# Optimization experiments

Measured on AMD Instinct MI355X. Metric: run time of the kernel, lower is better.

## Reference

```python
import jax, jax.numpy as jnp
import numpy as np

B, N, NVT, HS, GS, NZ, TE = 512, 32, 32, 512, 1024, 56, 3


def setup_inputs() -> dict:
    key = jax.random.key(0)
    ks = jax.random.split(key, 18)
    def w(k, shape, fan_in):
        return (jax.random.normal(k, shape, jnp.float32) / np.sqrt(fan_in)).astype(jnp.float32)
    node_types = jax.random.randint(ks[0], (B, N), 0, NVT, dtype=jnp.int32)
    # strictly upper-triangular random DAG: adj[b,u,v]=1 means edge u->v, u<v
    adj = ((jax.random.uniform(ks[1], (B, N, N)) < 0.15)
           & (jnp.triu(jnp.ones((N, N), bool), 1))).astype(jnp.float32)
    return {
        'node_types': node_types,
        'adj': adj,
        'finit_w': w(ks[2], (NVT + GS, HS), NVT + GS),
        'finit_b': w(ks[3], (HS,), HS),
        'fe_w':    w(ks[4], (2 * HS + 1, 2 * HS), 2 * HS + 1),
        'fe_b':    w(ks[5], (2 * HS,), 2 * HS),
        'grue_wih': w(ks[6], (TE, 3 * HS, 2 * HS), 2 * HS),
        'grue_whh': w(ks[7], (TE, 3 * HS, HS), HS),
        'grue_bih': w(ks[8], (TE, 3 * HS), HS),
        'grue_bhh': w(ks[9], (TE, 3 * HS), HS),
        'gate_w':  w(ks[10], (HS, GS), HS),
        'gate_b':  w(ks[11], (GS,), HS),
        'mapper_w': w(ks[12], (HS, GS), HS),
        'fc1_w':   w(ks[13], (GS, NZ), GS),
        'fc1_b':   w(ks[14], (NZ,), GS),
        'fc2_w':   w(ks[15], (GS, NZ), GS),
        'fc2_b':   w(ks[16], (NZ,), GS),
    }


def reference(node_types, adj, finit_w, finit_b, fe_w, fe_b,
              grue_wih, grue_whh, grue_bih, grue_bhh,
              gate_w, gate_b, mapper_w, fc1_w, fc1_b, fc2_w, fc2_b):
    # --- vertex init: finit(cat([one_hot(type), zeros(gs)])) -> only first NVT rows of finit_w matter
    X = jax.nn.one_hot(node_types, NVT, dtype=adj.dtype)          # [B,N,nvt]
    H = X @ finit_w[:NVT] + finit_b                                # [B,N,hs]

    deg = adj.sum(1)                                               # [B,N] in-degree of v
    # torch skips the fe+GRU update for vertex v only if NO graph in batch has a pred at v
    has_pred = (adj.sum((0, 1)) > 0)[None, :, None]                # [1,N,1]

    # fe(cat([H_u, e=1, H_v])) decomposed: W_nei@H_u + w_e + W_self@H_v + b, summed over preds
    Wn, we, Ws = fe_w[:HS], fe_w[HS], fe_w[HS + 1:]

    def step(H, p):
        wih, whh, bih, bhh = p
        Hu = H @ Wn                                                # [B,N,2hs]
        self_t = H @ Ws + we + fe_b                                # [B,N,2hs]
        # Av[b,v] = sum_u adj[b,u,v]*Hu[b,u] + deg[b,v]*self_t[b,v]
        Av = jnp.einsum('buv,bue->bve', adj, Hu) + deg[..., None] * self_t
        gx = Av @ wih.T + bih                                      # [B,N,3hs]
        gh = H @ whh.T + bhh                                       # [B,N,3hs]
        xr, xz, xn = jnp.split(gx, 3, -1)
        hr, hz, hn = jnp.split(gh, 3, -1)
        r = jax.nn.sigmoid(xr + hr)
        z = jax.nn.sigmoid(xz + hz)
        n = jnp.tanh(xn + r * hn)
        Hn = (1.0 - z) * n + z * H                                 # torch GRUCell
        return jnp.where(has_pred, Hn, H), None

    H, _ = jax.lax.scan(step, H, (grue_wih, grue_whh, grue_bih, grue_bhh))

    # gated graph readout: sum_v sigmoid(gate(Hv)) * mapper(Hv)
    Hg = (jax.nn.sigmoid(H @ gate_w + gate_b) * (H @ mapper_w)).sum(1)  # [B,gs]
    mu = Hg @ fc1_w + fc1_b
    logvar = Hg @ fc2_w + fc2_b
    return jnp.stack([mu, logvar], 0)                              # [2,B,nz]
```

## Files before the change

kernel.cpp:

```cpp
#include <hip/hip_runtime.h>
#include <hip/hip_bf16.h>

namespace {

constexpr int kB = 512, kN = 32, kHS = 512, kHS2 = 1024, kHS3 = 1536;
constexpr int kGS = 1024, kNZ = 56, kTE = 3;

typedef __attribute__((ext_vector_type(8))) short bf16x8;
typedef __attribute__((ext_vector_type(4))) float f32x4;

__device__ inline ushort f2bf(float f) {
    union { float f; unsigned u; } v; v.f = f;
    unsigned r = v.u + 0x7fffu + ((v.u >> 16) & 1u);
    return (ushort)(r >> 16);
}
__device__ inline float bf2f(ushort b) {
    union { unsigned u; float f; } v; v.u = ((unsigned)b) << 16;
    return v.f;
}

__global__ __launch_bounds__(256) void wnst_kernel(const float* __restrict__ fe_w,
    ushort* __restrict__ out)
{
    int idx = blockIdx.x * 256 + threadIdx.x;
    int n = idx >> 9, k = idx & 511;
    float v = (n < kHS2) ? fe_w[(size_t)k * kHS2 + n]
                         : fe_w[(size_t)(kHS + 1 + k) * kHS2 + (n - kHS2)];
    out[idx] = f2bf(v);
}

__global__ __launch_bounds__(256) void gatemap_kernel(const float* __restrict__ gw,
    const float* __restrict__ mw, ushort* __restrict__ out)
{
    int idx = blockIdx.x * 256 + threadIdx.x;
    int n = idx >> 9, k = idx & 511;
    float v = (n < kGS) ? gw[(size_t)k * kGS + n] : mw[(size_t)k * kGS + (n - kGS)];
    out[idx] = f2bf(v);
}

__global__ __launch_bounds__(256) void catrzn_kernel(const float* __restrict__ wih,
    const float* __restrict__ whh, ushort* __restrict__ out)
{
    int k = blockIdx.x * 256 + threadIdx.x;
    int n = blockIdx.y, t = blockIdx.z;
    float v;
    if (k < kHS2)       v = wih[((size_t)t * kHS3 + n) * kHS2 + k];
    else if (n < kHS2)  v = whh[((size_t)t * kHS3 + n) * kHS + (k - kHS2)];
    else                v = 0.f;
    out[((size_t)t * kHS3 + n) * kHS3 + k] = f2bf(v);
}

__global__ __launch_bounds__(256) void whhn_kernel(const float* __restrict__ whh,
    ushort* __restrict__ out)
{
    int k = blockIdx.x * 256 + threadIdx.x;
    int n = blockIdx.y, t = blockIdx.z;
    out[((size_t)t * kHS + n) * kHS + k] =
        f2bf(whh[((size_t)t * kHS3 + kHS2 + n) * kHS + k]);
}

__global__ __launch_bounds__(256) void deg_kernel(const float* __restrict__ adj,
    float* __restrict__ deg)
{
    int idx = blockIdx.x * 256 + threadIdx.x;
    int b = idx >> 5, v = idx & 31;
    const float* p = adj + (size_t)b * kN * kN + v;
    float s = 0.f;
    #pragma unroll
    for (int u = 0; u < kN; ++u) s += p[u * kN];
    deg[idx] = s;
}

__global__ void haspred_kernel(const float* __restrict__ deg, int* __restrict__ hp)
{
    int v = threadIdx.x;
    float s = 0.f;
    for (int b = 0; b < kB; ++b) s += deg[b * kN + v];
    hp[v] = (s > 0.f) ? 1 : 0;
}

__global__ void biasHS_kernel(const float* __restrict__ fe_w,
    const float* __restrict__ fe_b, float* __restrict__ o)
{
    int e = blockIdx.x * 256 + threadIdx.x;
    o[e] = (e < kHS2) ? 0.f
                      : fe_w[(size_t)kHS * kHS2 + (e - kHS2)] + fe_b[e - kHS2];
}

__global__ void biasGXN_kernel(const float* __restrict__ bih,
    const float* __restrict__ bhh, float* __restrict__ o)
{
    int idx = blockIdx.x * 256 + threadIdx.x;
    int t = idx / kHS3, e = idx % kHS3;
    float v = bih[t * kHS3 + e];
    if (e < kHS2) v += bhh[t * kHS3 + e];
    o[idx] = v;
}

__global__ void biasRO_kernel(const float* __restrict__ gb, float* __restrict__ o)
{
    int e = blockIdx.x * 256 + threadIdx.x;
    o[e] = (e < kGS) ? gb[e] : 0.f;
}

__global__ __launch_bounds__(256) void hinit_kernel(const int* __restrict__ nt,
    const float* __restrict__ finit_w, const float* __restrict__ finit_b,
    ushort* __restrict__ AvH)
{
    int idx = blockIdx.x * 256 + threadIdx.x;
    int m = idx >> 9;
    int h = idx & 511;
    int t = nt[m];
    AvH[(size_t)m * kHS3 + kHS2 + h] = f2bf(finit_w[t * kHS + h] + finit_b[h]);
}

template<typename CT>
__global__ __launch_bounds__(256, 2) void gemm_bf16(const ushort* __restrict__ A,
    const ushort* __restrict__ B, CT* __restrict__ C,
    const float* __restrict__ bias, int M_, int N_, int K_, int lda)
{
    __shared__ ushort smem[3 * 12288];
    const int tid = threadIdx.x;
    const int w = tid >> 6, l = tid & 63;
    const int l15 = l & 15;

    int nwg = gridDim.x * gridDim.y;
    int bid = blockIdx.y * gridDim.x + blockIdx.x;
    int swz = (nwg & 7) ? bid : ((bid & 7) * (nwg >> 3) + (bid >> 3));
    const int bx = swz % gridDim.x, by = swz / gridDim.x;
    const int mT = by * 128, nT = bx * 256;

    const int NT = K_ >> 5;

    auto stage = [&](const ushort* G, int ldg, int rowOff, int buf, int aOff,
                     int idx, int kt2) {
        int row = idx >> 2, sl = idx & 3;
        int gs = sl ^ ((row >> 1) & 3);
        const ushort* g = G + (size_t)(rowOff + row) * ldg + kt2 + gs * 8;
        __builtin_amdgcn_global_load_lds(
            (const __attribute__((address_space(1))) void*)g,
            (__attribute__((address_space(3))) void*)(smem + buf * 12288 + aOff + idx * 8),
            16, 0, 0);
    };
    auto stage_ph0 = [&](int t) {
        int buf = t % 3, kt2 = t * 32;
        stage(A, lda, mT, buf, 0, tid, kt2);
        stage(A, lda, mT, buf, 0, 256 + tid, kt2);
        stage(B, K_, nT, buf, 4096, tid, kt2);
    };
    auto stage_ph1 = [&](int t) {
        int buf = t % 3, kt2 = t * 32;
        stage(B, K_, nT, buf, 4096, 256 + tid, kt2);
        stage(B, K_, nT, buf, 4096, 512 + tid, kt2);
        stage(B, K_, nT, buf, 4096, 768 + tid, kt2);
    };

    f32x4 acc[8][4] = {};
    bf16x8 bfr[4];
    const int swd = ((l >> 4) ^ (l15 >> 1)) & 3;

    stage_ph0(0); stage_ph1(0);
    stage_ph0(1); stage_ph1(1);

    for (int t = 0; t < NT; ++t) {
        if (t + 1 < NT) asm volatile("s_waitcnt vmcnt(6)" ::: "memory");
        else            asm volatile("s_waitcnt vmcnt(0)" ::: "memory");
        __builtin_amdgcn_s_barrier();

        const ushort* Ab = smem + (t % 3) * 12288;
        const ushort* Bb = Ab + 4096;
        const bool st = (t + 2 < NT);

        bf16x8 af[4];
        #pragma unroll
        for (int i = 0; i < 4; ++i)
            af[i] = *reinterpret_cast<const bf16x8*>(
                &Ab[(i * 16 + l15) * 32 + swd * 8]);
        #pragma unroll
        for (int j = 0; j < 4; ++j)
            bfr[j] = *reinterpret_cast<const bf16x8*>(
                &Bb[(w * 64 + j * 16 + l15) * 32 + swd * 8]);
        if (st) stage_ph0(t + 2);
        asm volatile("s_waitcnt lgkmcnt(0)" ::: "memory");
        __builtin_amdgcn_sched_barrier(0);
        __builtin_amdgcn_s_setprio(1);
        #pragma unroll
        for (int i = 0; i < 4; ++i)
            #pragma unroll
            for (int j = 0; j < 4; ++j)
                acc[i][j] = __builtin_amdgcn_mfma_f32_16x16x32_bf16(
                    af[i], bfr[j], acc[i][j], 0, 0, 0);
        __builtin_amdgcn_s_setprio(0);
        __builtin_amdgcn_s_barrier();

        #pragma unroll
        for (int i = 0; i < 4; ++i)
            af[i] = *reinterpret_cast<const bf16x8*>(
                &Ab[((4 + i) * 16 + l15) * 32 + swd * 8]);
        if (st) stage_ph1(t + 2);
        asm volatile("s_waitcnt lgkmcnt(0)" ::: "memory");
        __builtin_amdgcn_sched_barrier(0);
        __builtin_amdgcn_s_setprio(1);
        #pragma unroll
        for (int i = 0; i < 4; ++i)
            #pragma unroll
            for (int j = 0; j < 4; ++j)
                acc[4 + i][j] = __builtin_amdgcn_mfma_f32_16x16x32_bf16(
                    af[i], bfr[j], acc[4 + i][j], 0, 0, 0);
        __builtin_amdgcn_s_setprio(0);
        __builtin_amdgcn_s_barrier();
    }

    const int row0 = (l >> 4) * 4;
    #pragma unroll
    for (int ni = 0; ni < 4; ++ni) {
        int col = nT + w * 64 + ni * 16 + l15;
        float bv = bias ? bias[col] : 0.f;
        #pragma unroll
        for (int mi = 0; mi < 8; ++mi) {
            #pragma unroll
            for (int q = 0; q < 4; ++q) {
                int row = mT + mi * 16 + row0 + q;
                float val = acc[mi][ni][q] + bv;
                if constexpr (sizeof(CT) == 2)
                    C[(size_t)row * N_ + col] = (CT)f2bf(val);
                else
                    C[(size_t)row * N_ + col] = (CT)val;
            }
        }
    }
}

template<typename CT>
void launch_gemm(const ushort* A, int lda, const ushort* B, CT* C,
                 const float* bias, int M_, int N_, int K_, hipStream_t stream)
{
    dim3 grid(N_ / 256, M_ / 128);
    gemm_bf16<CT><<<grid, 256, 0, stream>>>(A, B, C, bias, M_, N_, K_, lda);
}

__global__ __launch_bounds__(256) void av_kernel(const float* __restrict__ adj,
    const ushort* __restrict__ HuSt, const float* __restrict__ deg,
    ushort* __restrict__ AvH)
{
    __shared__ float adjs[kN * kN];
    __shared__ float degs[kN];
    int b = blockIdx.y;
    int e = blockIdx.x * 256 + threadIdx.x;
    {
        const float4* src = reinterpret_cast<const float4*>(adj + (size_t)b * kN * kN);
        float4 v = src[threadIdx.x];
        *reinterpret_cast<float4*>(&adjs[threadIdx.x * 4]) = v;
        if (threadIdx.x < kN) degs[threadIdx.x] = deg[b * kN + threadIdx.x];
    }
    __syncthreads();

    const size_t rbase = (size_t)b * kN * 2048 + e;
    float acc[kN];
    #pragma unroll
    for (int v = 0; v < kN; ++v)
        acc[v] = degs[v] * bf2f(HuSt[rbase + (size_t)v * 2048 + kHS2]);
    for (int u = 0; u < kN; ++u) {
        float hu = bf2f(HuSt[rbase + (size_t)u * 2048]);
        #pragma unroll
        for (int v4 = 0; v4 < kN / 4; ++v4) {
            float4 a = *reinterpret_cast<const float4*>(&adjs[u * kN + v4 * 4]);
            acc[v4 * 4 + 0] = fmaf(a.x, hu, acc[v4 * 4 + 0]);
            acc[v4 * 4 + 1] = fmaf(a.y, hu, acc[v4 * 4 + 1]);
            acc[v4 * 4 + 2] = fmaf(a.z, hu, acc[v4 * 4 + 2]);
            acc[v4 * 4 + 3] = fmaf(a.w, hu, acc[v4 * 4 + 3]);
        }
    }
    const size_t obase = (size_t)b * kN * kHS3 + e;
    #pragma unroll
    for (int v = 0; v < kN; ++v) AvH[obase + (size_t)v * kHS3] = f2bf(acc[v]);
}

__global__ __launch_bounds__(256) void gru_kernel(ushort* __restrict__ AvH,
    const ushort* __restrict__ gxzn, const ushort* __restrict__ hn,
    const int* __restrict__ hp)
{
    int idx = blockIdx.x * 256 + threadIdx.x;
    int m = idx >> 9;
    int h = idx & 511;
    size_t gb = (size_t)m * kHS3 + h;
    float rp = bf2f(gxzn[gb]);
    float zp = bf2f(gxzn[gb + kHS]);
    float xn = bf2f(gxzn[gb + 2 * kHS]);
    float hv = bf2f(hn[(size_t)m * kHS + h]);
    float r = 1.f / (1.f + __expf(-rp));
    float z = 1.f / (1.f + __expf(-zp));
    float n = tanhf(xn + r * hv);
    ushort* Hp = AvH + (size_t)m * kHS3 + kHS2 + h;
    float hold = bf2f(*Hp);
    float hnew = (1.f - z) * n + z * hold;
    *Hp = hp[m & 31] ? f2bf(hnew) : f2bf(hold);
}

__global__ __launch_bounds__(256) void hg_kernel(const float* __restrict__ G12,
    float* __restrict__ Hg)
{
    int idx = blockIdx.x * 256 + threadIdx.x;
    int b = idx >> 10, g = idx & 1023;
    size_t base = (size_t)b * kN * 2048 + g;
    float acc = 0.f;
    #pragma unroll 8
    for (int n = 0; n < kN; ++n) {
        float s  = G12[base + (size_t)n * 2048];
        float m2 = G12[base + (size_t)n * 2048 + kGS];
        float sig = 1.f / (1.f + __expf(-s));
        acc = fmaf(sig, m2, acc);
    }
    Hg[idx] = acc;
}

__global__ __launch_bounds__(64) void fc_kernel(const float* __restrict__ Hg,
    const float* __restrict__ fc1_w, const float* __restrict__ fc1_b,
    const float* __restrict__ fc2_w, const float* __restrict__ fc2_b,
    float* __restrict__ out, int b0)
{
    __shared__ float hg[kGS];
    int bl = blockIdx.x;
    for (int i = threadIdx.x; i < kGS; i += 64) hg[i] = Hg[(size_t)bl * kGS + i];
    __syncthreads();
    int j = threadIdx.x;
    if (j < kNZ) {
        float s1 = fc1_b[j], s2 = fc2_b[j];
        for (int k = 0; k < kGS; ++k) {
            float h = hg[k];
            s1 = fmaf(h, fc1_w[k * kNZ + j], s1);
            s2 = fmaf(h, fc2_w[k * kNZ + j], s2);
        }
        int bg = b0 + bl;
        out[(size_t)bg * kNZ + j] = s1;
        out[(size_t)kB * kNZ + (size_t)bg * kNZ + j] = s2;
    }
}

}

extern "C" void kernel_launch(void* const* d_in, const int* in_sizes, int n_in,
                              void* d_out, int out_size, void* d_ws, size_t ws_size,
                              hipStream_t stream)
{
    const int*   node_types = (const int*)  d_in[0];
    const float* adj        = (const float*)d_in[1];
    const float* finit_w    = (const float*)d_in[2];
    const float* finit_b    = (const float*)d_in[3];
    const float* fe_w       = (const float*)d_in[4];
    const float* fe_b       = (const float*)d_in[5];
    const float* grue_wih   = (const float*)d_in[6];
    const float* grue_whh   = (const float*)d_in[7];
    const float* grue_bih   = (const float*)d_in[8];
    const float* grue_bhh   = (const float*)d_in[9];
    const float* gate_w     = (const float*)d_in[10];
    const float* gate_b     = (const float*)d_in[11];
    const float* mapper_w   = (const float*)d_in[12];
    const float* fc1_w      = (const float*)d_in[13];
    const float* fc1_b      = (const float*)d_in[14];
    const float* fc2_w      = (const float*)d_in[15];
    const float* fc2_b      = (const float*)d_in[16];
    float* out = (float*)d_out;

    float* W = (float*)d_ws;
    size_t o = 0;
    float*  deg     = W + o; o += (size_t)kB * kN;
    int*    hp      = (int*)(W + o); o += 64;
    float*  biasHS  = W + o; o += 2048;
    float*  biasGXN = W + o; o += kTE * kHS3;
    float*  biasRO  = W + o; o += 2048;
    float*  Hg      = W + o; o += (size_t)kB * kGS;
    ushort* WnsT    = (ushort*)(W + o); o += (size_t)2048 * kHS / 2;
    ushort* catRZN  = (ushort*)(W + o); o += (size_t)kTE * kHS3 * kHS3 / 2;
    ushort* whhN    = (ushort*)(W + o); o += (size_t)kTE * kHS * kHS / 2;
    ushort* gateMapT= (ushort*)(W + o); o += (size_t)2048 * kHS / 2;
    const size_t fixedFloats = o;

    const size_t perGraph = 90112;
    int CH = 512;
    while (CH > 4 &&
           (fixedFloats + (size_t)CH * perGraph) * sizeof(float) > ws_size)
        CH >>= 1;

    deg_kernel<<<kB * kN / 256, 256, 0, stream>>>(adj, deg);
    haspred_kernel<<<1, kN, 0, stream>>>(deg, hp);
    biasHS_kernel<<<2048 / 256, 256, 0, stream>>>(fe_w, fe_b, biasHS);
    biasGXN_kernel<<<kTE * kHS3 / 256, 256, 0, stream>>>(grue_bih, grue_bhh, biasGXN);
    biasRO_kernel<<<2048 / 256, 256, 0, stream>>>(gate_b, biasRO);
    wnst_kernel<<<2048 * kHS / 256, 256, 0, stream>>>(fe_w, WnsT);
    catrzn_kernel<<<dim3(kHS3 / 256, kHS3, kTE), 256, 0, stream>>>(grue_wih, grue_whh, catRZN);
    whhn_kernel<<<dim3(kHS / 256, kHS, kTE), 256, 0, stream>>>(grue_whh, whhN);
    gatemap_kernel<<<2048 * kHS / 256, 256, 0, stream>>>(gate_w, mapper_w, gateMapT);

    for (int b0 = 0; b0 < kB; b0 += CH) {
        const int MC = CH * kN;
        ushort* AvH  = (ushort*)(W + fixedFloats);
        ushort* HuSt = AvH  + (size_t)MC * kHS3;
        ushort* gxzn = HuSt + (size_t)MC * 2048;
        ushort* hnb  = gxzn + (size_t)MC * kHS3;
        float*  G12  = (float*)HuSt;
        ushort* Hc   = AvH + kHS2;

        hinit_kernel<<<MC * kHS / 256, 256, 0, stream>>>(
            node_types + (size_t)b0 * kN, finit_w, finit_b, AvH);

        for (int t = 0; t < kTE; ++t) {
            launch_gemm<ushort>(Hc, kHS3, WnsT, HuSt, biasHS, MC, 2048, kHS, stream);
            {
                dim3 g(kHS2 / 256, CH);
                av_kernel<<<g, 256, 0, stream>>>(
                    adj + (size_t)b0 * kN * kN, HuSt, deg + (size_t)b0 * kN, AvH);
            }
            launch_gemm<ushort>(AvH, kHS3, catRZN + (size_t)t * kHS3 * kHS3, gxzn,
                                biasGXN + t * kHS3, MC, kHS3, kHS3, stream);
            launch_gemm<ushort>(Hc, kHS3, whhN + (size_t)t * kHS * kHS, hnb,
                                grue_bhh + t * kHS3 + kHS2, MC, kHS, kHS, stream);
            gru_kernel<<<MC * kHS / 256, 256, 0, stream>>>(AvH, gxzn, hnb, hp);
        }

        launch_gemm<float>(Hc, kHS3, gateMapT, G12, biasRO, MC, 2048, kHS, stream);
        hg_kernel<<<CH * kGS / 256, 256, 0, stream>>>(G12, Hg);
        fc_kernel<<<CH, 64, 0, stream>>>(Hg, fc1_w, fc1_b, fc2_w, fc2_b, out, b0);
    }
}
```

Baseline: 870.0 us.

## Precompose fe and GRU input weights so each step runs one wide GEMM

Folds the fe linear layer into the GRU input projection by precomputing Wih·Wn and Wih·Ws products once per timestep. Each step then runs a single H×[4608×512] GEMM that yields the neighbour, self and hidden gate pre-activations. The adjacency mixing moves onto the 1536-wide projected features, and the degree-scaled self terms and biases are applied inside the gate kernel. This trades the K=1536 gate GEMM and the separate Whh GEMM for a wider single GEMM plus a setup cost. It changes bf16 rounding order, because composed weights are rounded to bf16, and the mixer now reads a wider tensor.

New measurement: 973.7 us. 11.9% more time.

```diff
diff --git a/kernel.cpp b/kernel.cpp
--- a/kernel.cpp
+++ b/kernel.cpp
@@ -5,6 +5,7 @@
 
 constexpr int kB = 512, kN = 32, kHS = 512, kHS2 = 1024, kHS3 = 1536;
 constexpr int kGS = 1024, kNZ = 56, kTE = 3;
+constexpr int kNC = 4608;
 
 typedef __attribute__((ext_vector_type(8))) short bf16x8;
 typedef __attribute__((ext_vector_type(4))) float f32x4;
@@ -19,14 +20,11 @@
     return v.f;
 }
 
-__global__ __launch_bounds__(256) void wnst_kernel(const float* __restrict__ fe_w,
-    ushort* __restrict__ out)
-{
-    int idx = blockIdx.x * 256 + threadIdx.x;
-    int n = idx >> 9, k = idx & 511;
-    float v = (n < kHS2) ? fe_w[(size_t)k * kHS2 + n]
-                         : fe_w[(size_t)(kHS + 1 + k) * kHS2 + (n - kHS2)];
-    out[idx] = f2bf(v);
+__global__ __launch_bounds__(256) void copybf_kernel(const float* __restrict__ in,
+    ushort* __restrict__ out, int n)
+{
+    int i = blockIdx.x * 256 + threadIdx.x;
+    if (i < n) out[i] = f2bf(in[i]);
 }
 
 __global__ __launch_bounds__(256) void gatemap_kernel(const float* __restrict__ gw,
@@ -36,27 +34,6 @@
     int n = idx >> 9, k = idx & 511;
     float v = (n < kGS) ? gw[(size_t)k * kGS + n] : mw[(size_t)k * kGS + (n - kGS)];
     out[idx] = f2bf(v);
-}
-
-__global__ __launch_bounds__(256) void catrzn_kernel(const float* __restrict__ wih,
-    const float* __restrict__ whh, ushort* __restrict__ out)
-{
-    int k = blockIdx.x * 256 + threadIdx.x;
-    int n = blockIdx.y, t = blockIdx.z;
-    float v;
-    if (k < kHS2)       v = wih[((size_t)t * kHS3 + n) * kHS2 + k];
-    else if (n < kHS2)  v = whh[((size_t)t * kHS3 + n) * kHS + (k - kHS2)];
-    else                v = 0.f;
-    out[((size_t)t * kHS3 + n) * kHS3 + k] = f2bf(v);
-}
-
-__global__ __launch_bounds__(256) void whhn_kernel(const float* __restrict__ whh,
-    ushort* __restrict__ out)
-{
-    int k = blockIdx.x * 256 + threadIdx.x;
-    int n = blockIdx.y, t = blockIdx.z;
-    out[((size_t)t * kHS + n) * kHS + k] =
-        f2bf(whh[((size_t)t * kHS3 + kHS2 + n) * kHS + k]);
 }
 
 __global__ __launch_bounds__(256) void deg_kernel(const float* __restrict__ adj,
@@ -79,22 +56,22 @@
     hp[v] = (s > 0.f) ? 1 : 0;
 }
 
-__global__ void biasHS_kernel(const float* __restrict__ fe_w,
+__global__ void be_kernel(const float* __restrict__ fe_w,
     const float* __restrict__ fe_b, float* __restrict__ o)
 {
-    int e = blockIdx.x * 256 + threadIdx.x;
-    o[e] = (e < kHS2) ? 0.f
-                      : fe_w[(size_t)kHS * kHS2 + (e - kHS2)] + fe_b[e - kHS2];
-}
-
-__global__ void biasGXN_kernel(const float* __restrict__ bih,
-    const float* __restrict__ bhh, float* __restrict__ o)
+    int j = blockIdx.x * 256 + threadIdx.x;
+    o[j] = fe_w[(size_t)kHS * kHS2 + j] + fe_b[j];
+}
+
+__global__ __launch_bounds__(256) void bewih_kernel(const float* __restrict__ be,
+    const float* __restrict__ wih, float* __restrict__ o)
 {
     int idx = blockIdx.x * 256 + threadIdx.x;
     int t = idx / kHS3, e = idx % kHS3;
-    float v = bih[t * kHS3 + e];
-    if (e < kHS2) v += bhh[t * kHS3 + e];
-    o[idx] = v;
+    const float* wr = wih + ((size_t)t * kHS3 + e) * kHS2;
+    float s = 0.f;
+    for (int j = 0; j < kHS2; ++j) s = fmaf(be[j], wr[j], s);
+    o[idx] = s;
 }
 
 __global__ void biasRO_kernel(const float* __restrict__ gb, float* __restrict__ o)
@@ -105,13 +82,13 @@
 
 __global__ __launch_bounds__(256) void hinit_kernel(const int* __restrict__ nt,
     const float* __restrict__ finit_w, const float* __restrict__ finit_b,
-    ushort* __restrict__ AvH)
+    ushort* __restrict__ H)
 {
     int idx = blockIdx.x * 256 + threadIdx.x;
     int m = idx >> 9;
     int h = idx & 511;
     int t = nt[m];
-    AvH[(size_t)m * kHS3 + kHS2 + h] = f2bf(finit_w[t * kHS + h] + finit_b[h]);
+    H[idx] = f2bf(finit_w[t * kHS + h] + finit_b[h]);
 }
 
 template<typename CT>
@@ -239,62 +216,66 @@
     gemm_bf16<CT><<<grid, 256, 0, stream>>>(A, B, C, bias, M_, N_, K_, lda);
 }
 
-__global__ __launch_bounds__(256) void av_kernel(const float* __restrict__ adj,
-    const ushort* __restrict__ HuSt, const float* __restrict__ deg,
-    ushort* __restrict__ AvH)
+__global__ __launch_bounds__(256) void mixer_kernel(const float* __restrict__ adj,
+    const ushort* __restrict__ P, ushort* __restrict__ AP)
 {
     __shared__ float adjs[kN * kN];
-    __shared__ float degs[kN];
     int b = blockIdx.y;
     int e = blockIdx.x * 256 + threadIdx.x;
     {
         const float4* src = reinterpret_cast<const float4*>(adj + (size_t)b * kN * kN);
         float4 v = src[threadIdx.x];
         *reinterpret_cast<float4*>(&adjs[threadIdx.x * 4]) = v;
-        if (threadIdx.x < kN) degs[threadIdx.x] = deg[b * kN + threadIdx.x];
     }
     __syncthreads();
 
-    const size_t rbase = (size_t)b * kN * 2048 + e;
+    const size_t rbase = (size_t)b * kN * kNC + e;
     float acc[kN];
     #pragma unroll
-    for (int v = 0; v < kN; ++v)
-        acc[v] = degs[v] * bf2f(HuSt[rbase + (size_t)v * 2048 + kHS2]);
+    for (int v = 0; v < kN; ++v) acc[v] = 0.f;
     for (int u = 0; u < kN; ++u) {
-        float hu = bf2f(HuSt[rbase + (size_t)u * 2048]);
+        float pu = bf2f(P[rbase + (size_t)u * kNC]);
         #pragma unroll
         for (int v4 = 0; v4 < kN / 4; ++v4) {
             float4 a = *reinterpret_cast<const float4*>(&adjs[u * kN + v4 * 4]);
-            acc[v4 * 4 + 0] = fmaf(a.x, hu, acc[v4 * 4 + 0]);
-            acc[v4 * 4 + 1] = fmaf(a.y, hu, acc[v4 * 4 + 1]);
-            acc[v4 * 4 + 2] = fmaf(a.z, hu, acc[v4 * 4 + 2]);
-            acc[v4 * 4 + 3] = fmaf(a.w, hu, acc[v4 * 4 + 3]);
+            acc[v4 * 4 + 0] = fmaf(a.x, pu, acc[v4 * 4 + 0]);
+            acc[v4 * 4 + 1] = fmaf(a.y, pu, acc[v4 * 4 + 1]);
+            acc[v4 * 4 + 2] = fmaf(a.z, pu, acc[v4 * 4 + 2]);
+            acc[v4 * 4 + 3] = fmaf(a.w, pu, acc[v4 * 4 + 3]);
         }
     }
     const size_t obase = (size_t)b * kN * kHS3 + e;
     #pragma unroll
-    for (int v = 0; v < kN; ++v) AvH[obase + (size_t)v * kHS3] = f2bf(acc[v]);
-}
-
-__global__ __launch_bounds__(256) void gru_kernel(ushort* __restrict__ AvH,
-    const ushort* __restrict__ gxzn, const ushort* __restrict__ hn,
+    for (int v = 0; v < kN; ++v) AP[obase + (size_t)v * kHS3] = f2bf(acc[v]);
+}
+
+__global__ __launch_bounds__(256) void gate_kernel(ushort* __restrict__ H,
+    const ushort* __restrict__ AP, const ushort* __restrict__ P,
+    const float* __restrict__ degc, const float* __restrict__ bewih,
+    const float* __restrict__ bih, const float* __restrict__ bhh,
     const int* __restrict__ hp)
 {
     int idx = blockIdx.x * 256 + threadIdx.x;
     int m = idx >> 9;
     int h = idx & 511;
-    size_t gb = (size_t)m * kHS3 + h;
-    float rp = bf2f(gxzn[gb]);
-    float zp = bf2f(gxzn[gb + kHS]);
-    float xn = bf2f(gxzn[gb + 2 * kHS]);
-    float hv = bf2f(hn[(size_t)m * kHS + h]);
-    float r = 1.f / (1.f + __expf(-rp));
-    float z = 1.f / (1.f + __expf(-zp));
-    float n = tanhf(xn + r * hv);
-    ushort* Hp = AvH + (size_t)m * kHS3 + kHS2 + h;
-    float hold = bf2f(*Hp);
+    float dm = degc[m];
+    const size_t ap = (size_t)m * kHS3 + h;
+    const size_t pv = (size_t)m * kNC + kHS3 + h;
+    const size_t pw = (size_t)m * kNC + 2 * kHS3 + h;
+
+    float gxr = bf2f(AP[ap])            + dm * (bf2f(P[pv])            + bewih[h])            + bih[h];
+    float gxz = bf2f(AP[ap + kHS])      + dm * (bf2f(P[pv + kHS])      + bewih[h + kHS])      + bih[h + kHS];
+    float gxn = bf2f(AP[ap + 2 * kHS])  + dm * (bf2f(P[pv + 2 * kHS])  + bewih[h + 2 * kHS])  + bih[h + 2 * kHS];
+    float ghr = bf2f(P[pw])           + bhh[h];
+    float ghz = bf2f(P[pw + kHS])     + bhh[h + kHS];
+    float ghn = bf2f(P[pw + 2 * kHS]) + bhh[h + 2 * kHS];
+
+    float r = 1.f / (1.f + __expf(-(gxr + ghr)));
+    float z = 1.f / (1.f + __expf(-(gxz + ghz)));
+    float n = tanhf(gxn + r * ghn);
+    float hold = bf2f(H[idx]);
     float hnew = (1.f - z) * n + z * hold;
-    *Hp = hp[m & 31] ? f2bf(hnew) : f2bf(hold);
+    H[idx] = hp[m & 31] ? f2bf(hnew) : f2bf(hold);
 }
 
 __global__ __launch_bounds__(256) void hg_kernel(const float* __restrict__ G12,
@@ -366,59 +347,80 @@
     size_t o = 0;
     float*  deg     = W + o; o += (size_t)kB * kN;
     int*    hp      = (int*)(W + o); o += 64;
-    float*  biasHS  = W + o; o += 2048;
-    float*  biasGXN = W + o; o += kTE * kHS3;
+    float*  be      = W + o; o += kHS2;
+    float*  bewih   = W + o; o += kTE * kHS3;
     float*  biasRO  = W + o; o += 2048;
     float*  Hg      = W + o; o += (size_t)kB * kGS;
-    ushort* WnsT    = (ushort*)(W + o); o += (size_t)2048 * kHS / 2;
-    ushort* catRZN  = (ushort*)(W + o); o += (size_t)kTE * kHS3 * kHS3 / 2;
-    ushort* whhN    = (ushort*)(W + o); o += (size_t)kTE * kHS * kHS / 2;
     ushort* gateMapT= (ushort*)(W + o); o += (size_t)2048 * kHS / 2;
+    ushort* COMB    = (ushort*)(W + o); o += (size_t)kTE * kNC * kHS / 2;
     const size_t fixedFloats = o;
 
-    const size_t perGraph = 90112;
+    const size_t perGraph = 106496;
     int CH = 512;
     while (CH > 4 &&
            (fixedFloats + (size_t)CH * perGraph) * sizeof(float) > ws_size)
         CH >>= 1;
 
+    float* chunkBase = W + fixedFloats;
+
+    ushort* wihB = (ushort*)chunkBase;
+    ushort* WnB  = wihB + (size_t)kTE * kHS3 * kHS2;
+    ushort* WsB  = WnB  + (size_t)kHS * kHS2;
+
     deg_kernel<<<kB * kN / 256, 256, 0, stream>>>(adj, deg);
     haspred_kernel<<<1, kN, 0, stream>>>(deg, hp);
-    biasHS_kernel<<<2048 / 256, 256, 0, stream>>>(fe_w, fe_b, biasHS);
-    biasGXN_kernel<<<kTE * kHS3 / 256, 256, 0, stream>>>(grue_bih, grue_bhh, biasGXN);
+    be_kernel<<<kHS2 / 256, 256, 0, stream>>>(fe_w, fe_b, be);
+    bewih_kernel<<<kTE * kHS3 / 256, 256, 0, stream>>>(be, grue_wih, bewih);
     biasRO_kernel<<<2048 / 256, 256, 0, stream>>>(gate_b, biasRO);
-    wnst_kernel<<<2048 * kHS / 256, 256, 0, stream>>>(fe_w, WnsT);
-    catrzn_kernel<<<dim3(kHS3 / 256, kHS3, kTE), 256, 0, stream>>>(grue_wih, grue_whh, catRZN);
-    whhn_kernel<<<dim3(kHS / 256, kHS, kTE), 256, 0, stream>>>(grue_whh, whhN);
     gatemap_kernel<<<2048 * kHS / 256, 256, 0, stream>>>(gate_w, mapper_w, gateMapT);
+
+    {
+        int n1 = kTE * kHS3 * kHS2;
+        copybf_kernel<<<(n1 + 255) / 256, 256, 0, stream>>>(grue_wih, wihB, n1);
+        int n2 = kHS * kHS2;
+        copybf_kernel<<<(n2 + 255) / 256, 256, 0, stream>>>(fe_w, WnB, n2);
+        copybf_kernel<<<(n2 + 255) / 256, 256, 0, stream>>>(
+            fe_w + (size_t)(kHS + 1) * kHS2, WsB, n2);
+        int n3 = kHS3 * kHS;
+        for (int t = 0; t < kTE; ++t)
+            copybf_kernel<<<(n3 + 255) / 256, 256, 0, stream>>>(
+                grue_whh + (size_t)t * n3,
+                COMB + ((size_t)t * kNC + 2 * kHS3) * kHS, n3);
+    }
+    for (int t = 0; t < kTE; ++t) {
+        const ushort* At = wihB + (size_t)t * kHS3 * kHS2;
+        launch_gemm<ushort>(At, kHS2, WnB,
+                            COMB + (size_t)t * kNC * kHS, nullptr,
+                            kHS3, kHS, kHS2, stream);
+        launch_gemm<ushort>(At, kHS2, WsB,
+                            COMB + ((size_t)t * kNC + kHS3) * kHS, nullptr,
+                            kHS3, kHS, kHS2, stream);
+    }
 
     for (int b0 = 0; b0 < kB; b0 += CH) {
         const int MC = CH * kN;
-        ushort* AvH  = (ushort*)(W + fixedFloats);
-        ushort* HuSt = AvH  + (size_t)MC * kHS3;
-        ushort* gxzn = HuSt + (size_t)MC * 2048;
-        ushort* hnb  = gxzn + (size_t)MC * kHS3;
-        float*  G12  = (float*)HuSt;
-        ushort* Hc   = AvH + kHS2;
+        ushort* P  = (ushort*)chunkBase;
+        ushort* AP = P  + (size_t)MC * kNC;
+        ushort* H  = AP + (size_t)MC * kHS3;
+        float*  G12 = (float*)P;
 
         hinit_kernel<<<MC * kHS / 256, 256, 0, stream>>>(
-            node_types + (size_t)b0 * kN, finit_w, finit_b, AvH);
+            node_types + (size_t)b0 * kN, finit_w, finit_b, H);
 
         for (int t = 0; t < kTE; ++t) {
-            launch_gemm<ushort>(Hc, kHS3, WnsT, HuSt, biasHS, MC, 2048, kHS, stream);
+            launch_gemm<ushort>(H, kHS, COMB + (size_t)t * kNC * kHS, P,
+                                nullptr, MC, kNC, kHS, stream);
             {
-                dim3 g(kHS2 / 256, CH);
-                av_kernel<<<g, 256, 0, stream>>>(
-                    adj + (size_t)b0 * kN * kN, HuSt, deg + (size_t)b0 * kN, AvH);
+                dim3 g(kHS3 / 256, CH);
+                mixer_kernel<<<g, 256, 0, stream>>>(
+                    adj + (size_t)b0 * kN * kN, P, AP);
             }
-            launch_gemm<ushort>(AvH, kHS3, catRZN + (size_t)t * kHS3 * kHS3, gxzn,
-                                biasGXN + t * kHS3, MC, kHS3, kHS3, stream);
-            launch_gemm<ushort>(Hc, kHS3, whhN + (size_t)t * kHS * kHS, hnb,
-                                grue_bhh + t * kHS3 + kHS2, MC, kHS, kHS, stream);
-            gru_kernel<<<MC * kHS / 256, 256, 0, stream>>>(AvH, gxzn, hnb, hp);
+            gate_kernel<<<MC * kHS / 256, 256, 0, stream>>>(
+                H, AP, P, deg + (size_t)b0 * kN, bewih + (size_t)t * kHS3,
+                grue_bih + (size_t)t * kHS3, grue_bhh + (size_t)t * kHS3, hp);
         }
 
-        launch_gemm<float>(Hc, kHS3, gateMapT, G12, biasRO, MC, 2048, kHS, stream);
+        launch_gemm<float>(H, kHS, gateMapT, G12, biasRO, MC, 2048, kHS, stream);
         hg_kernel<<<CH * kGS / 256, 256, 0, stream>>>(G12, Hg);
         fc_kernel<<<CH, 64, 0, stream>>>(Hg, fc1_w, fc1_b, fc2_w, fc2_b, out, b0);
     }
```

## Load GEMM B operand directly into registers, 2x2 wave tiling, LDS only for A

Applied to the files above, without the earlier changes.

The GEMM kernel stops staging the B (weight) tile through LDS. Each wave now loads its B fragments straight from global memory into two register banks that are double-buffered across k-steps, and only A is staged through LDS. Waves are rearranged into a 2x2 grid of 64x128 sub-tiles, and the block swizzle now walks M first so that neighbouring blocks share B columns. The aim is to cut LDS traffic and footprint, at the cost of higher register pressure and uncoalesced 16-byte-per-lane global loads for B. The hand-tuned vmcnt waits must match the exact number of loads in flight.

Measured after the change: 1.289 ms. 48.1% more time.

```diff
diff --git a/kernel.cpp b/kernel.cpp
--- a/kernel.cpp
+++ b/kernel.cpp
@@ -119,109 +119,135 @@
     const ushort* __restrict__ B, CT* __restrict__ C,
     const float* __restrict__ bias, int M_, int N_, int K_, int lda)
 {
-    __shared__ ushort smem[3 * 12288];
+    __shared__ ushort As[3 * 4096];
     const int tid = threadIdx.x;
     const int w = tid >> 6, l = tid & 63;
     const int l15 = l & 15;
+    const int wm = w >> 1, wn = w & 1;
 
     int nwg = gridDim.x * gridDim.y;
     int bid = blockIdx.y * gridDim.x + blockIdx.x;
     int swz = (nwg & 7) ? bid : ((bid & 7) * (nwg >> 3) + (bid >> 3));
-    const int bx = swz % gridDim.x, by = swz / gridDim.x;
+    const int by = swz % gridDim.y, bx = swz / gridDim.y;
     const int mT = by * 128, nT = bx * 256;
 
     const int NT = K_ >> 5;
 
-    auto stage = [&](const ushort* G, int ldg, int rowOff, int buf, int aOff,
-                     int idx, int kt2) {
-        int row = idx >> 2, sl = idx & 3;
-        int gs = sl ^ ((row >> 1) & 3);
-        const ushort* g = G + (size_t)(rowOff + row) * ldg + kt2 + gs * 8;
-        __builtin_amdgcn_global_load_lds(
-            (const __attribute__((address_space(1))) void*)g,
-            (__attribute__((address_space(3))) void*)(smem + buf * 12288 + aOff + idx * 8),
-            16, 0, 0);
+    auto stageA = [&](int t) {
+        int buf = t % 3, kt2 = t * 32;
+        #pragma unroll
+        for (int i = 0; i < 2; ++i) {
+            int idx = tid + i * 256;
+            int row = idx >> 2, sl = idx & 3;
+            int gs = sl ^ ((row >> 1) & 3);
+            const ushort* g = A + (size_t)(mT + row) * lda + kt2 + gs * 8;
+            __builtin_amdgcn_global_load_lds(
+                (const __attribute__((address_space(1))) void*)g,
+                (__attribute__((address_space(3))) void*)(As + buf * 4096 + idx * 8),
+                16, 0, 0);
+        }
     };
-    auto stage_ph0 = [&](int t) {
-        int buf = t % 3, kt2 = t * 32;
-        stage(A, lda, mT, buf, 0, tid, kt2);
-        stage(A, lda, mT, buf, 0, 256 + tid, kt2);
-        stage(B, K_, nT, buf, 4096, tid, kt2);
-    };
-    auto stage_ph1 = [&](int t) {
-        int buf = t % 3, kt2 = t * 32;
-        stage(B, K_, nT, buf, 4096, 256 + tid, kt2);
-        stage(B, K_, nT, buf, 4096, 512 + tid, kt2);
-        stage(B, K_, nT, buf, 4096, 768 + tid, kt2);
-    };
-
-    f32x4 acc[8][4] = {};
-    bf16x8 bfr[4];
+
+    const ushort* bp0 = B + (size_t)(nT + wn * 128 +  0 + l15) * K_ + (l >> 4) * 8;
+    const ushort* bp1 = B + (size_t)(nT + wn * 128 + 16 + l15) * K_ + (l >> 4) * 8;
+    const ushort* bp2 = B + (size_t)(nT + wn * 128 + 32 + l15) * K_ + (l >> 4) * 8;
+    const ushort* bp3 = B + (size_t)(nT + wn * 128 + 48 + l15) * K_ + (l >> 4) * 8;
+    const ushort* bp4 = B + (size_t)(nT + wn * 128 + 64 + l15) * K_ + (l >> 4) * 8;
+    const ushort* bp5 = B + (size_t)(nT + wn * 128 + 80 + l15) * K_ + (l >> 4) * 8;
+    const ushort* bp6 = B + (size_t)(nT + wn * 128 + 96 + l15) * K_ + (l >> 4) * 8;
+    const ushort* bp7 = B + (size_t)(nT + wn * 128 + 112 + l15) * K_ + (l >> 4) * 8;
+
+    bf16x8 bA[8], bB[8];
+    #define LOAD_BANK(bank)                                            \
+        do {                                                           \
+            bank[0] = *reinterpret_cast<const bf16x8*>(bp0); bp0 += 32;\
+            bank[1] = *reinterpret_cast<const bf16x8*>(bp1); bp1 += 32;\
+            bank[2] = *reinterpret_cast<const bf16x8*>(bp2); bp2 += 32;\
+            bank[3] = *reinterpret_cast<const bf16x8*>(bp3); bp3 += 32;\
+            bank[4] = *reinterpret_cast<const bf16x8*>(bp4); bp4 += 32;\
+            bank[5] = *reinterpret_cast<const bf16x8*>(bp5); bp5 += 32;\
+            bank[6] = *reinterpret_cast<const bf16x8*>(bp6); bp6 += 32;\
+            bank[7] = *reinterpret_cast<const bf16x8*>(bp7); bp7 += 32;\
+        } while (0)
+
+    f32x4 acc[4][8] = {};
     const int swd = ((l >> 4) ^ (l15 >> 1)) & 3;
 
-    stage_ph0(0); stage_ph1(0);
-    stage_ph0(1); stage_ph1(1);
-
-    for (int t = 0; t < NT; ++t) {
-        if (t + 1 < NT) asm volatile("s_waitcnt vmcnt(6)" ::: "memory");
-        else            asm volatile("s_waitcnt vmcnt(0)" ::: "memory");
+    stageA(0);
+    stageA(1);
+    LOAD_BANK(bA);
+
+    bf16x8 af[4];
+    #define DS_AF(t)                                                         \
+        do {                                                                 \
+            const ushort* Ab_ = As + ((t) % 3) * 4096;                       \
+            _Pragma("unroll")                                                \
+            for (int mi = 0; mi < 4; ++mi)                                   \
+                af[mi] = *reinterpret_cast<const bf16x8*>(                   \
+                    &Ab_[(wm * 64 + mi * 16 + l15) * 32 + swd * 8]);         \
+        } while (0)
+
+    #define MFMA_ALL(bank)                                                   \
+        do {                                                                 \
+            __builtin_amdgcn_s_setprio(1);                                   \
+            _Pragma("unroll")                                                \
+            for (int mi = 0; mi < 4; ++mi)                                   \
+                _Pragma("unroll")                                            \
+                for (int nj = 0; nj < 8; ++nj)                               \
+                    acc[mi][nj] = __builtin_amdgcn_mfma_f32_16x16x32_bf16(   \
+                        af[mi], bank[nj], acc[mi][nj], 0, 0, 0);             \
+            __builtin_amdgcn_s_setprio(0);                                   \
+        } while (0)
+
+    int t = 0;
+    for (; t + 2 < NT - 1; t += 2) {
+        asm volatile("s_waitcnt vmcnt(10)" ::: "memory");
         __builtin_amdgcn_s_barrier();
-
-        const ushort* Ab = smem + (t % 3) * 12288;
-        const ushort* Bb = Ab + 4096;
-        const bool st = (t + 2 < NT);
-
-        bf16x8 af[4];
-        #pragma unroll
-        for (int i = 0; i < 4; ++i)
-            af[i] = *reinterpret_cast<const bf16x8*>(
-                &Ab[(i * 16 + l15) * 32 + swd * 8]);
-        #pragma unroll
-        for (int j = 0; j < 4; ++j)
-            bfr[j] = *reinterpret_cast<const bf16x8*>(
-                &Bb[(w * 64 + j * 16 + l15) * 32 + swd * 8]);
-        if (st) stage_ph0(t + 2);
-        asm volatile("s_waitcnt lgkmcnt(0)" ::: "memory");
+        DS_AF(t);
+        LOAD_BANK(bB);
+        stageA(t + 2);
+        asm volatile("s_waitcnt vmcnt(12) lgkmcnt(0)" ::: "memory");
         __builtin_amdgcn_sched_barrier(0);
-        __builtin_amdgcn_s_setprio(1);
-        #pragma unroll
-        for (int i = 0; i < 4; ++i)
-            #pragma unroll
-            for (int j = 0; j < 4; ++j)
-                acc[i][j] = __builtin_amdgcn_mfma_f32_16x16x32_bf16(
-                    af[i], bfr[j], acc[i][j], 0, 0, 0);
-        __builtin_amdgcn_s_setprio(0);
+        MFMA_ALL(bA);
+
+        asm volatile("s_waitcnt vmcnt(10)" ::: "memory");
         __builtin_amdgcn_s_barrier();
-
-        #pragma unroll
-        for (int i = 0; i < 4; ++i)
-            af[i] = *reinterpret_cast<const bf16x8*>(
-                &Ab[((4 + i) * 16 + l15) * 32 + swd * 8]);
-        if (st) stage_ph1(t + 2);
-        asm volatile("s_waitcnt lgkmcnt(0)" ::: "memory");
+        DS_AF(t + 1);
+        LOAD_BANK(bA);
+        stageA(t + 3);
+        asm volatile("s_waitcnt vmcnt(12) lgkmcnt(0)" ::: "memory");
         __builtin_amdgcn_sched_barrier(0);
-        __builtin_amdgcn_s_setprio(1);
-        #pragma unroll
-        for (int i = 0; i < 4; ++i)
-            #pragma unroll
-            for (int j = 0; j < 4; ++j)
-                acc[4 + i][j] = __builtin_amdgcn_mfma_f32_16x16x32_bf16(
-                    af[i], bfr[j], acc[4 + i][j], 0, 0, 0);
-        __builtin_amdgcn_s_setprio(0);
-        __builtin_amdgcn_s_barrier();
-    }
+        MFMA_ALL(bB);
+    }
+    asm volatile("s_waitcnt vmcnt(10)" ::: "memory");
+    __builtin_amdgcn_s_barrier();
+    DS_AF(NT - 2);
+    LOAD_BANK(bB);
+    asm volatile("s_waitcnt vmcnt(10) lgkmcnt(0)" ::: "memory");
+    __builtin_amdgcn_sched_barrier(0);
+    MFMA_ALL(bA);
+    asm volatile("s_waitcnt vmcnt(8)" ::: "memory");
+    __builtin_amdgcn_s_barrier();
+    DS_AF(NT - 1);
+    asm volatile("s_waitcnt vmcnt(0) lgkmcnt(0)" ::: "memory");
+    __builtin_amdgcn_sched_barrier(0);
+    MFMA_ALL(bB);
+
+    #undef LOAD_BANK
+    #undef DS_AF
+    #undef MFMA_ALL
 
     const int row0 = (l >> 4) * 4;
     #pragma unroll
-    for (int ni = 0; ni < 4; ++ni) {
-        int col = nT + w * 64 + ni * 16 + l15;
+    for (int nj = 0; nj < 8; ++nj) {
+        int col = nT + wn * 128 + nj * 16 + l15;
         float bv = bias ? bias[col] : 0.f;
         #pragma unroll
-        for (int mi = 0; mi < 8; ++mi) {
+        for (int mi = 0; mi < 4; ++mi) {
             #pragma unroll
             for (int q = 0; q < 4; ++q) {
-                int row = mT + mi * 16 + row0 + q;
-                float val = acc[mi][ni][q] + bv;
+                int row = mT + wm * 64 + mi * 16 + row0 + q;
+                float val = acc[mi][nj][q] + bv;
                 if constexpr (sizeof(CT) == 2)
                     C[(size_t)row * N_ + col] = (CT)f2bf(val);
                 else
```

## Merge hidden-gate GEMM into combined GRU GEMM and enlarge GEMM tile

Applied to the files above, without the earlier changes.

The separate W_hh n-gate GEMM is folded into the combined GRU-gate GEMM. The weight matrix gets 512 extra output rows that read only the H part of the input, with zeros in the Av columns. The GEMM kernel moves to 512 threads and 256x256 tiles with double buffering, and staging is interleaved between the MFMA blocks. This removes a kernel launch and a second read of H, and raises data reuse per tile. In exchange it does extra zero-multiply work over the K=1024 Av columns for the hn output, and the larger block may lower occupancy.

Result: slower. 914.4 us (+5.1%).

```diff
diff --git a/kernel.cpp b/kernel.cpp
--- a/kernel.cpp
+++ b/kernel.cpp
@@ -38,25 +38,22 @@
     out[idx] = f2bf(v);
 }
 
-__global__ __launch_bounds__(256) void catrzn_kernel(const float* __restrict__ wih,
+__global__ __launch_bounds__(256) void catrznh_kernel(const float* __restrict__ wih,
     const float* __restrict__ whh, ushort* __restrict__ out)
 {
     int k = blockIdx.x * 256 + threadIdx.x;
     int n = blockIdx.y, t = blockIdx.z;
     float v;
-    if (k < kHS2)       v = wih[((size_t)t * kHS3 + n) * kHS2 + k];
-    else if (n < kHS2)  v = whh[((size_t)t * kHS3 + n) * kHS + (k - kHS2)];
-    else                v = 0.f;
-    out[((size_t)t * kHS3 + n) * kHS3 + k] = f2bf(v);
-}
-
-__global__ __launch_bounds__(256) void whhn_kernel(const float* __restrict__ whh,
-    ushort* __restrict__ out)
-{
-    int k = blockIdx.x * 256 + threadIdx.x;
-    int n = blockIdx.y, t = blockIdx.z;
-    out[((size_t)t * kHS + n) * kHS + k] =
-        f2bf(whh[((size_t)t * kHS3 + kHS2 + n) * kHS + k]);
+    if (n < kHS3) {
+        if (k < kHS2)       v = wih[((size_t)t * kHS3 + n) * kHS2 + k];
+        else if (n < kHS2)  v = whh[((size_t)t * kHS3 + n) * kHS + (k - kHS2)];
+        else                v = 0.f;
+    } else {
+        v = (k >= kHS2)
+          ? whh[((size_t)t * kHS3 + kHS2 + (n - kHS3)) * kHS + (k - kHS2)]
+          : 0.f;
+    }
+    out[((size_t)t * 2048 + n) * kHS3 + k] = f2bf(v);
 }
 
 __global__ __launch_bounds__(256) void deg_kernel(const float* __restrict__ adj,
@@ -87,13 +84,15 @@
                       : fe_w[(size_t)kHS * kHS2 + (e - kHS2)] + fe_b[e - kHS2];
 }
 
-__global__ void biasGXN_kernel(const float* __restrict__ bih,
+__global__ void biasGXNH_kernel(const float* __restrict__ bih,
     const float* __restrict__ bhh, float* __restrict__ o)
 {
     int idx = blockIdx.x * 256 + threadIdx.x;
-    int t = idx / kHS3, e = idx % kHS3;
-    float v = bih[t * kHS3 + e];
-    if (e < kHS2) v += bhh[t * kHS3 + e];
+    int t = idx >> 11, e = idx & 2047;
+    float v;
+    if (e < kHS2)      v = bih[t * kHS3 + e] + bhh[t * kHS3 + e];
+    else if (e < kHS3) v = bih[t * kHS3 + e];
+    else               v = bhh[t * kHS3 + (e - 512)];
     o[idx] = v;
 }
 
@@ -115,113 +114,134 @@
 }
 
 template<typename CT>
-__global__ __launch_bounds__(256, 2) void gemm_bf16(const ushort* __restrict__ A,
+__global__ __launch_bounds__(512, 2) void gemm_bf16(const ushort* __restrict__ A,
     const ushort* __restrict__ B, CT* __restrict__ C,
     const float* __restrict__ bias, int M_, int N_, int K_, int lda)
 {
-    __shared__ ushort smem[3 * 12288];
+    __shared__ ushort smem[32768];
     const int tid = threadIdx.x;
     const int w = tid >> 6, l = tid & 63;
     const int l15 = l & 15;
+    const int wm = w >> 2, wn = w & 3;
+    const int khi = l >> 4;
 
     int nwg = gridDim.x * gridDim.y;
     int bid = blockIdx.y * gridDim.x + blockIdx.x;
     int swz = (nwg & 7) ? bid : ((bid & 7) * (nwg >> 3) + (bid >> 3));
     const int bx = swz % gridDim.x, by = swz / gridDim.x;
-    const int mT = by * 128, nT = bx * 256;
+    const int mT = by * 256, nT = bx * 256;
 
     const int NT = K_ >> 5;
 
-    auto stage = [&](const ushort* G, int ldg, int rowOff, int buf, int aOff,
-                     int idx, int kt2) {
-        int row = idx >> 2, sl = idx & 3;
-        int gs = sl ^ ((row >> 1) & 3);
-        const ushort* g = G + (size_t)(rowOff + row) * ldg + kt2 + gs * 8;
-        __builtin_amdgcn_global_load_lds(
-            (const __attribute__((address_space(1))) void*)g,
-            (__attribute__((address_space(3))) void*)(smem + buf * 12288 + aOff + idx * 8),
-            16, 0, 0);
+    auto stageA = [&](int t) {
+        int p = t & 1, kt = t * 32;
+        #pragma unroll
+        for (int r = 0; r < 2; ++r) {
+            int idx = r * 512 + tid;
+            int row = idx >> 2, sl = idx & 3;
+            int gs = sl ^ ((row >> 1) & 3);
+            const ushort* g = A + (size_t)(mT + row) * lda + kt + gs * 8;
+            __builtin_amdgcn_global_load_lds(
+                (const __attribute__((address_space(1))) void*)g,
+                (__attribute__((address_space(3))) void*)(smem + p * 8192 + idx * 8),
+                16, 0, 0);
+        }
     };
-    auto stage_ph0 = [&](int t) {
-        int buf = t % 3, kt2 = t * 32;
-        stage(A, lda, mT, buf, 0, tid, kt2);
-        stage(A, lda, mT, buf, 0, 256 + tid, kt2);
-        stage(B, K_, nT, buf, 4096, tid, kt2);
+    auto stageB = [&](int t) {
+        int p = t & 1, kt = t * 32;
+        #pragma unroll
+        for (int r = 0; r < 2; ++r) {
+            int idx = r * 512 + tid;
+            int row = idx >> 2, sl = idx & 3;
+            int gs = sl ^ ((row >> 1) & 3);
+            const ushort* g = B + (size_t)(nT + row) * K_ + kt + gs * 8;
+            __builtin_amdgcn_global_load_lds(
+                (const __attribute__((address_space(1))) void*)g,
+                (__attribute__((address_space(3))) void*)(smem + 16384 + p * 8192 + idx * 8),
+                16, 0, 0);
+        }
     };
-    auto stage_ph1 = [&](int t) {
-        int buf = t % 3, kt2 = t * 32;
-        stage(B, K_, nT, buf, 4096, 256 + tid, kt2);
-        stage(B, K_, nT, buf, 4096, 512 + tid, kt2);
-        stage(B, K_, nT, buf, 4096, 768 + tid, kt2);
+
+    f32x4 acc[8][4] = {};
+    bf16x8 af[4], bfr[4];
+    const int ps = (khi ^ (l15 >> 1)) & 3;
+
+    auto dsA = [&](int p, int mb) {
+        const ushort* base = smem + p * 8192;
+        #pragma unroll
+        for (int mi = 0; mi < 4; ++mi) {
+            int ra = wm * 128 + (mb + mi) * 16 + l15;
+            af[mi] = *reinterpret_cast<const bf16x8*>(base + ra * 32 + ps * 8);
+        }
     };
-
-    f32x4 acc[8][4] = {};
-    bf16x8 bfr[4];
-    const int swd = ((l >> 4) ^ (l15 >> 1)) & 3;
-
-    stage_ph0(0); stage_ph1(0);
-    stage_ph0(1); stage_ph1(1);
+    auto dsB = [&](int p) {
+        const ushort* base = smem + 16384 + p * 8192;
+        #pragma unroll
+        for (int nj = 0; nj < 4; ++nj) {
+            int rb = wn * 64 + nj * 16 + l15;
+            bfr[nj] = *reinterpret_cast<const bf16x8*>(base + rb * 32 + ps * 8);
+        }
+    };
+
+    stageA(0); stageB(0);
+    stageA(1); stageB(1);
 
     for (int t = 0; t < NT; ++t) {
-        if (t + 1 < NT) asm volatile("s_waitcnt vmcnt(6)" ::: "memory");
+        const int p = t & 1;
+        if (t + 1 < NT) asm volatile("s_waitcnt vmcnt(4)" ::: "memory");
         else            asm volatile("s_waitcnt vmcnt(0)" ::: "memory");
         __builtin_amdgcn_s_barrier();
 
-        const ushort* Ab = smem + (t % 3) * 12288;
-        const ushort* Bb = Ab + 4096;
-        const bool st = (t + 2 < NT);
-
-        bf16x8 af[4];
-        #pragma unroll
-        for (int i = 0; i < 4; ++i)
-            af[i] = *reinterpret_cast<const bf16x8*>(
-                &Ab[(i * 16 + l15) * 32 + swd * 8]);
-        #pragma unroll
-        for (int j = 0; j < 4; ++j)
-            bfr[j] = *reinterpret_cast<const bf16x8*>(
-                &Bb[(w * 64 + j * 16 + l15) * 32 + swd * 8]);
-        if (st) stage_ph0(t + 2);
+        dsA(p, 0);
+        dsB(p);
         asm volatile("s_waitcnt lgkmcnt(0)" ::: "memory");
         __builtin_amdgcn_sched_barrier(0);
         __builtin_amdgcn_s_setprio(1);
         #pragma unroll
-        for (int i = 0; i < 4; ++i)
+        for (int mi = 0; mi < 4; ++mi)
             #pragma unroll
-            for (int j = 0; j < 4; ++j)
-                acc[i][j] = __builtin_amdgcn_mfma_f32_16x16x32_bf16(
-                    af[i], bfr[j], acc[i][j], 0, 0, 0);
+            for (int nj = 0; nj < 4; ++nj)
+                acc[mi][nj] = __builtin_amdgcn_mfma_f32_16x16x32_bf16(
+                    af[mi], bfr[nj], acc[mi][nj], 0, 0, 0);
         __builtin_amdgcn_s_setprio(0);
-        __builtin_amdgcn_s_barrier();
-
-        #pragma unroll
-        for (int i = 0; i < 4; ++i)
-            af[i] = *reinterpret_cast<const bf16x8*>(
-                &Ab[((4 + i) * 16 + l15) * 32 + swd * 8]);
-        if (st) stage_ph1(t + 2);
+
+        dsA(p, 4);
         asm volatile("s_waitcnt lgkmcnt(0)" ::: "memory");
         __builtin_amdgcn_sched_barrier(0);
+        __builtin_amdgcn_s_barrier();
+
+        const bool st = (t + 2 < NT);
+        if (st) stageA(t + 2);
         __builtin_amdgcn_s_setprio(1);
         #pragma unroll
-        for (int i = 0; i < 4; ++i)
+        for (int mi = 0; mi < 4; ++mi)
             #pragma unroll
-            for (int j = 0; j < 4; ++j)
-                acc[4 + i][j] = __builtin_amdgcn_mfma_f32_16x16x32_bf16(
-                    af[i], bfr[j], acc[4 + i][j], 0, 0, 0);
+            for (int nj = 0; nj < 2; ++nj)
+                acc[4 + mi][nj] = __builtin_amdgcn_mfma_f32_16x16x32_bf16(
+                    af[mi], bfr[nj], acc[4 + mi][nj], 0, 0, 0);
         __builtin_amdgcn_s_setprio(0);
-        __builtin_amdgcn_s_barrier();
-    }
-
-    const int row0 = (l >> 4) * 4;
+        if (st) stageB(t + 2);
+        __builtin_amdgcn_s_setprio(1);
+        #pragma unroll
+        for (int mi = 0; mi < 4; ++mi)
+            #pragma unroll
+            for (int nj = 2; nj < 4; ++nj)
+                acc[4 + mi][nj] = __builtin_amdgcn_mfma_f32_16x16x32_bf16(
+                    af[mi], bfr[nj], acc[4 + mi][nj], 0, 0, 0);
+        __builtin_amdgcn_s_setprio(0);
+    }
+
+    const int row0 = khi * 4;
     #pragma unroll
-    for (int ni = 0; ni < 4; ++ni) {
-        int col = nT + w * 64 + ni * 16 + l15;
+    for (int nj = 0; nj < 4; ++nj) {
+        int col = nT + wn * 64 + nj * 16 + l15;
         float bv = bias ? bias[col] : 0.f;
         #pragma unroll
         for (int mi = 0; mi < 8; ++mi) {
             #pragma unroll
             for (int q = 0; q < 4; ++q) {
-                int row = mT + mi * 16 + row0 + q;
-                float val = acc[mi][ni][q] + bv;
+                int row = mT + wm * 128 + mi * 16 + row0 + q;
+                float val = acc[mi][nj][q] + bv;
                 if constexpr (sizeof(CT) == 2)
                     C[(size_t)row * N_ + col] = (CT)f2bf(val);
                 else
@@ -235,8 +255,8 @@
 void launch_gemm(const ushort* A, int lda, const ushort* B, CT* C,
                  const float* bias, int M_, int N_, int K_, hipStream_t stream)
 {
-    dim3 grid(N_ / 256, M_ / 128);
-    gemm_bf16<CT><<<grid, 256, 0, stream>>>(A, B, C, bias, M_, N_, K_, lda);
+    dim3 grid(N_ / 256, M_ / 256);
+    gemm_bf16<CT><<<grid, 512, 0, stream>>>(A, B, C, bias, M_, N_, K_, lda);
 }
 
 __global__ __launch_bounds__(256) void av_kernel(const float* __restrict__ adj,
@@ -277,17 +297,16 @@
 }
 
 __global__ __launch_bounds__(256) void gru_kernel(ushort* __restrict__ AvH,
-    const ushort* __restrict__ gxzn, const ushort* __restrict__ hn,
-    const int* __restrict__ hp)
+    const ushort* __restrict__ gxznh, const int* __restrict__ hp)
 {
     int idx = blockIdx.x * 256 + threadIdx.x;
     int m = idx >> 9;
     int h = idx & 511;
-    size_t gb = (size_t)m * kHS3 + h;
-    float rp = bf2f(gxzn[gb]);
-    float zp = bf2f(gxzn[gb + kHS]);
-    float xn = bf2f(gxzn[gb + 2 * kHS]);
-    float hv = bf2f(hn[(size_t)m * kHS + h]);
+    const ushort* g = gxznh + (size_t)m * 2048;
+    float rp = bf2f(g[h]);
+    float zp = bf2f(g[h + 512]);
+    float xn = bf2f(g[h + 1024]);
+    float hv = bf2f(g[h + 1536]);
     float r = 1.f / (1.f + __expf(-rp));
     float z = 1.f / (1.f + __expf(-zp));
     float n = tanhf(xn + r * hv);
@@ -364,42 +383,39 @@
 
     float* W = (float*)d_ws;
     size_t o = 0;
-    float*  deg     = W + o; o += (size_t)kB * kN;
-    int*    hp      = (int*)(W + o); o += 64;
-    float*  biasHS  = W + o; o += 2048;
-    float*  biasGXN = W + o; o += kTE * kHS3;
-    float*  biasRO  = W + o; o += 2048;
-    float*  Hg      = W + o; o += (size_t)kB * kGS;
-    ushort* WnsT    = (ushort*)(W + o); o += (size_t)2048 * kHS / 2;
-    ushort* catRZN  = (ushort*)(W + o); o += (size_t)kTE * kHS3 * kHS3 / 2;
-    ushort* whhN    = (ushort*)(W + o); o += (size_t)kTE * kHS * kHS / 2;
-    ushort* gateMapT= (ushort*)(W + o); o += (size_t)2048 * kHS / 2;
+    float*  deg      = W + o; o += (size_t)kB * kN;
+    int*    hp       = (int*)(W + o); o += 64;
+    float*  biasHS   = W + o; o += 2048;
+    float*  biasGXNH = W + o; o += kTE * 2048;
+    float*  biasRO   = W + o; o += 2048;
+    float*  Hg       = W + o; o += (size_t)kB * kGS;
+    ushort* WnsT     = (ushort*)(W + o); o += (size_t)2048 * kHS / 2;
+    ushort* catRZNH  = (ushort*)(W + o); o += (size_t)kTE * 2048 * kHS3 / 2;
+    ushort* gateMapT = (ushort*)(W + o); o += (size_t)2048 * kHS / 2;
     const size_t fixedFloats = o;
 
     const size_t perGraph = 90112;
     int CH = 512;
-    while (CH > 4 &&
+    while (CH > 8 &&
            (fixedFloats + (size_t)CH * perGraph) * sizeof(float) > ws_size)
         CH >>= 1;
 
     deg_kernel<<<kB * kN / 256, 256, 0, stream>>>(adj, deg);
     haspred_kernel<<<1, kN, 0, stream>>>(deg, hp);
     biasHS_kernel<<<2048 / 256, 256, 0, stream>>>(fe_w, fe_b, biasHS);
-    biasGXN_kernel<<<kTE * kHS3 / 256, 256, 0, stream>>>(grue_bih, grue_bhh, biasGXN);
+    biasGXNH_kernel<<<kTE * 2048 / 256, 256, 0, stream>>>(grue_bih, grue_bhh, biasGXNH);
     biasRO_kernel<<<2048 / 256, 256, 0, stream>>>(gate_b, biasRO);
     wnst_kernel<<<2048 * kHS / 256, 256, 0, stream>>>(fe_w, WnsT);
-    catrzn_kernel<<<dim3(kHS3 / 256, kHS3, kTE), 256, 0, stream>>>(grue_wih, grue_whh, catRZN);
-    whhn_kernel<<<dim3(kHS / 256, kHS, kTE), 256, 0, stream>>>(grue_whh, whhN);
+    catrznh_kernel<<<dim3(kHS3 / 256, 2048, kTE), 256, 0, stream>>>(grue_wih, grue_whh, catRZNH);
     gatemap_kernel<<<2048 * kHS / 256, 256, 0, stream>>>(gate_w, mapper_w, gateMapT);
 
     for (int b0 = 0; b0 < kB; b0 += CH) {
         const int MC = CH * kN;
-        ushort* AvH  = (ushort*)(W + fixedFloats);
-        ushort* HuSt = AvH  + (size_t)MC * kHS3;
-        ushort* gxzn = HuSt + (size_t)MC * 2048;
-        ushort* hnb  = gxzn + (size_t)MC * kHS3;
-        float*  G12  = (float*)HuSt;
-        ushort* Hc   = AvH + kHS2;
+        ushort* AvH   = (ushort*)(W + fixedFloats);
+        ushort* HuSt  = AvH   + (size_t)MC * kHS3;
+        ushort* gxznh = HuSt  + (size_t)MC * 2048;
+        float*  G12   = (float*)HuSt;
+        ushort* Hc    = AvH + kHS2;
 
         hinit_kernel<<<MC * kHS / 256, 256, 0, stream>>>(
             node_types + (size_t)b0 * kN, finit_w, finit_b, AvH);
@@ -411,11 +427,9 @@
                 av_kernel<<<g, 256, 0, stream>>>(
                     adj + (size_t)b0 * kN * kN, HuSt, deg + (size_t)b0 * kN, AvH);
             }
-            launch_gemm<ushort>(AvH, kHS3, catRZN + (size_t)t * kHS3 * kHS3, gxzn,
-                                biasGXN + t * kHS3, MC, kHS3, kHS3, stream);
-            launch_gemm<ushort>(Hc, kHS3, whhN + (size_t)t * kHS * kHS, hnb,
-                                grue_bhh + t * kHS3 + kHS2, MC, kHS, kHS, stream);
-            gru_kernel<<<MC * kHS / 256, 256, 0, stream>>>(AvH, gxzn, hnb, hp);
+            launch_gemm<ushort>(AvH, kHS3, catRZNH + (size_t)t * 2048 * kHS3, gxznh,
+                                biasGXNH + t * 2048, MC, 2048, kHS3, stream);
+            gru_kernel<<<MC * kHS / 256, 256, 0, stream>>>(AvH, gxznh, hp);
         }
 
         launch_gemm<float>(Hc, kHS3, gateMapT, G12, biasRO, MC, 2048, kHS, stream);
```
